# Kernel optimization log

Measured on AMD Instinct MI355X. Metric: run time of the kernel, lower is better.

## Reference

```python
import jax, jax.numpy as jnp
import numpy as np

B, N = 8, 1000
EMB, K, F1E, F1V, MSG = 4, 3, 2, 3, 2


def cross_concat(h):
    # h: [b, n, d] -> [b, n, n, 2d], interleaving (h_i, h_j) per feature (stack axis=-1 then reshape)
    b, n, d = h.shape
    hi = jnp.broadcast_to(h[:, :, None, :], (b, n, n, d))
    hj = jnp.broadcast_to(h[:, None, :, :], (b, n, n, d))
    return jnp.stack((hi, hj), axis=-1).reshape(b, n, n, 2 * d)


def setup_inputs() -> dict:
    key = jax.random.key(0)
    ks = jax.random.split(key, 16)
    p = lambda k, s: (jax.random.normal(k, s, dtype=jnp.float32) * 0.1)
    return {
        "x": jax.random.normal(ks[0], (B, N), dtype=jnp.float32),
        "W1_emb": p(ks[1], (1, EMB)), "b1_emb": p(ks[2], (EMB,)),
        "W2_emb": p(ks[3], (1, EMB)), "b2_emb": p(ks[4], (EMB,)),
        "W_f1e": p(ks[5], (2 * EMB, F1E)), "b_f1e": p(ks[6], (F1E,)),
        "W_f2e": p(ks[7], (2 * F1V, K)), "b_f2e": p(ks[8], (K,)),
        "W_fk": p(ks[9], (K, 2 * EMB, MSG)), "b_fk": p(ks[10], (K, MSG)),
        "W_f1v": p(ks[11], (F1E, F1V)), "b_f1v": p(ks[12], (F1V,)),
        "W_f2v": p(ks[13], (MSG + 1, 1)), "b_f2v": p(ks[14], (1,)),
    }


def reference(x, W1_emb, b1_emb, W2_emb, b2_emb, W_f1e, b_f1e, W_f2e, b_f2e,
              W_fk, b_fk, W_f1v, b_f1v, W_f2v, b_f2v):
    x_ = x[..., None]                                  # [B,N,1]
    h1 = x_ @ W1_emb + b1_emb                          # [B,N,EMB]
    c = cross_concat(h1)                               # [B,N,N,2*EMB]
    h = jnp.sum(c @ W_f1e + b_f1e, axis=2)             # [B,N,F1E]
    h2 = h @ W_f1v + b_f1v                             # [B,N,F1V]
    c2 = cross_concat(h2)                              # [B,N,N,2*F1V]
    hsum = jnp.sum(c2, axis=0)                         # [N,N,2*F1V] (sum over batch)
    edge_logits = hsum @ W_f2e + b_f2e                 # [N,N,K]
    edge_probs = jax.nn.softmax(edge_logits, axis=-1)  # [N,N,K]
    h1_ = x_ @ W2_emb + b2_emb                         # [B,N,EMB]
    c3 = cross_concat(h1_)                             # [B,N,N,2*EMB]
    # K per-relation edge MLPs, stacked on the last axis -> [B,N,N,MSG,K]
    messages = jnp.einsum('bijd,kdm->bijmk', c3, W_fk) + b_fk.T
    # softmax-weighted combine, summed over receiver axis j and relation axis k
    v_e = jnp.einsum('ijk,bijmk->bim', edge_probs, messages)  # [B,N,MSG]
    h2_ = x_ + (jnp.concatenate((v_e, x_), axis=-1) @ W_f2v + b_f2v)
    return jnp.squeeze(h2_, axis=-1)                   # [B,N]
```

## Files before the change

kernel.cpp:

```cpp
#include <hip/hip_runtime.h>

#define NN 1000
#define BB 8


__device__ __forceinline__ float wave_sum(float v) {
#pragma unroll
    for (int o = 32; o > 0; o >>= 1) v += __shfl_xor(v, o, 64);
    return v;
}

__global__ void prep_kernel(const float* __restrict__ x,
                            const float* __restrict__ W1, const float* __restrict__ b1,
                            const float* __restrict__ W2, const float* __restrict__ b2,
                            const float* __restrict__ Wf1e, const float* __restrict__ bf1e,
                            const float* __restrict__ Wf2e, const float* __restrict__ bf2e,
                            const float* __restrict__ Wfk, const float* __restrict__ bfk,
                            const float* __restrict__ Wf1v, const float* __restrict__ bf1v,
                            const float* __restrict__ Wf2v, const float* __restrict__ bf2v,
                            float* __restrict__ ws) {
    float* rec = ws;
    float* Ai  = ws + 12 * NN;
    float* XsT = ws + 16 * NN;
    float* cst = ws + 17 * NN;
    const int tid = threadIdx.x;

    __shared__ float s_part[4][8];
    __shared__ float s_small[6];

    float sx[8] = {0, 0, 0, 0, 0, 0, 0, 0};
    for (int j = tid; j < NN; j += 256) {
        float xs = 0.f;
#pragma unroll
        for (int b = 0; b < 8; ++b) {
            float v = x[b * NN + j];
            rec[j * 12 + 4 + b] = v;
            sx[b] += v;
            xs += v;
        }
        XsT[j] = xs;
    }
#pragma unroll
    for (int b = 0; b < 8; ++b) {
        float v = wave_sum(sx[b]);
        if ((tid & 63) == 0) s_part[tid >> 6][b] = v;
    }
    __syncthreads();

    if (tid == 0) {
        float Sx[8];
#pragma unroll
        for (int b = 0; b < 8; ++b)
            Sx[b] = s_part[0][b] + s_part[1][b] + s_part[2][b] + s_part[3][b];

        float alpha[2];
        for (int f = 0; f < 2; ++f) {
            float a = 0.f;
            for (int e = 0; e < 4; ++e) a += W1[e] * Wf1e[(2 * e) * 2 + f];
            alpha[f] = (float)NN * a;
        }
        float gamma[3];
        for (int v = 0; v < 3; ++v) {
            float g = 0.f;
            for (int f = 0; f < 2; ++f) g += alpha[f] * Wf1v[f * 3 + v];
            gamma[v] = g;
        }
        float Ds[3] = {0.f, 0.f, 0.f};
        for (int b = 0; b < 8; ++b) {
            float S1e[4];
            for (int e = 0; e < 4; ++e) S1e[e] = Sx[b] * W1[e] + (float)NN * b1[e];
            float beta[2];
            for (int f = 0; f < 2; ++f) {
                float t = 0.f;
                for (int e = 0; e < 4; ++e) t += b1[e] * Wf1e[(2 * e) * 2 + f];
                t *= (float)NN;
                for (int e = 0; e < 4; ++e) t += S1e[e] * Wf1e[(2 * e + 1) * 2 + f];
                t += (float)NN * bf1e[f];
                beta[f] = t;
            }
            for (int v = 0; v < 3; ++v) {
                float d = bf1v[v];
                for (int f = 0; f < 2; ++f) d += beta[f] * Wf1v[f * 3 + v];
                Ds[v] += d;
            }
        }
        for (int v = 0; v < 3; ++v) { s_small[v] = gamma[v]; s_small[3 + v] = Ds[v]; }

        for (int m = 0; m < 2; ++m)
            for (int k = 0; k < 3; ++k) {
                float uA = 0.f, uB = 0.f, vA = 0.f, vB = 0.f;
                for (int e = 0; e < 4; ++e) {
                    float wE = Wfk[k * 16 + (2 * e) * 2 + m];
                    float wO = Wfk[k * 16 + (2 * e + 1) * 2 + m];
                    uA += W2[e] * wE; uB += b2[e] * wE;
                    vA += W2[e] * wO; vB += b2[e] * wO;
                }
                cst[m * 3 + k]      = uA;
                cst[6 + m * 3 + k]  = uB + bfk[k * 2 + m] + vB;
                cst[12 + m * 3 + k] = vA;
            }
        cst[18] = Wf2v[0]; cst[19] = Wf2v[1]; cst[20] = Wf2v[2]; cst[21] = bf2v[0];
    }
    __syncthreads();

    const float g0 = s_small[0], g1 = s_small[1], g2 = s_small[2];
    const float d0 = s_small[3], d1 = s_small[4], d2 = s_small[5];
    for (int j = tid; j < NN; j += 256) {
        float xs = XsT[j];
        float H0 = g0 * xs + d0, H1 = g1 * xs + d1, H2 = g2 * xs + d2;
#pragma unroll
        for (int k = 0; k < 3; ++k) {
            Ai[j * 4 + k]   = H0 * Wf2e[0 * 3 + k] + H1 * Wf2e[2 * 3 + k] + H2 * Wf2e[4 * 3 + k] + bf2e[k];
            rec[j * 12 + k] = H0 * Wf2e[1 * 3 + k] + H1 * Wf2e[3 * 3 + k] + H2 * Wf2e[5 * 3 + k];
        }
        Ai[j * 4 + 3] = 0.f;
        rec[j * 12 + 3] = 0.f;
    }
}

__global__ __launch_bounds__(64) void main_kernel(const float* __restrict__ ws,
                                                  float* __restrict__ out) {
    const float* rec = ws;
    const float* Ai  = ws + 12 * NN;
    const float* cst = ws + 17 * NN;
    const int i = blockIdx.x;
    const int t = threadIdx.x;

    const float4 aif = *reinterpret_cast<const float4*>(Ai + i * 4);
    const float ai0 = aif.x, ai1 = aif.y, ai2 = aif.z;

    float Q0 = 0.f, Q1 = 0.f, Q2 = 0.f;
    float R[8][3];
#pragma unroll
    for (int b = 0; b < 8; ++b)
#pragma unroll
        for (int k = 0; k < 3; ++k) R[b][k] = 0.f;

    for (int j = t; j < NN; j += 64) {
        const float4 a  = *reinterpret_cast<const float4*>(rec + j * 12);
        const float4 xA = *reinterpret_cast<const float4*>(rec + j * 12 + 4);
        const float4 xB = *reinterpret_cast<const float4*>(rec + j * 12 + 8);
        float l0 = ai0 + a.x, l1 = ai1 + a.y, l2 = ai2 + a.z;
        float mx = fmaxf(l0, fmaxf(l1, l2));
        float e0 = __expf(l0 - mx), e1 = __expf(l1 - mx), e2 = __expf(l2 - mx);
        float inv = 1.f / (e0 + e1 + e2);
        float p0 = e0 * inv, p1 = e1 * inv, p2 = e2 * inv;
        Q0 += p0; Q1 += p1; Q2 += p2;
        float xv[8] = {xA.x, xA.y, xA.z, xA.w, xB.x, xB.y, xB.z, xB.w};
#pragma unroll
        for (int b = 0; b < 8; ++b) {
            R[b][0] += p0 * xv[b];
            R[b][1] += p1 * xv[b];
            R[b][2] += p2 * xv[b];
        }
    }

    Q0 = wave_sum(Q0); Q1 = wave_sum(Q1); Q2 = wave_sum(Q2);
#pragma unroll
    for (int b = 0; b < 8; ++b) {
        R[b][0] = wave_sum(R[b][0]);
        R[b][1] = wave_sum(R[b][1]);
        R[b][2] = wave_sum(R[b][2]);
    }

    if (t == 0) {
        float uA[6], cB[6], vA[6];
#pragma unroll
        for (int q = 0; q < 6; ++q) { uA[q] = cst[q]; cB[q] = cst[6 + q]; vA[q] = cst[12 + q]; }
        float w0 = cst[18], w1 = cst[19], w2 = cst[20], bf = cst[21];
        float Q[3] = {Q0, Q1, Q2};
#pragma unroll
        for (int b = 0; b < 8; ++b) {
            float xi = rec[i * 12 + 4 + b];
            float ve[2];
#pragma unroll
            for (int m = 0; m < 2; ++m) {
                float s = 0.f;
#pragma unroll
                for (int k = 0; k < 3; ++k)
                    s += Q[k] * (uA[m * 3 + k] * xi + cB[m * 3 + k]) + vA[m * 3 + k] * R[b][k];
                ve[m] = s;
            }
            out[b * NN + i] = xi + ve[0] * w0 + ve[1] * w1 + xi * w2 + bf;
        }
    }
}

extern "C" void kernel_launch(void* const* d_in, const int* in_sizes, int n_in,
                              void* d_out, int out_size, void* d_ws, size_t ws_size,
                              hipStream_t stream) {
    const float* x    = (const float*)d_in[0];
    const float* W1   = (const float*)d_in[1];
    const float* b1   = (const float*)d_in[2];
    const float* W2   = (const float*)d_in[3];
    const float* b2   = (const float*)d_in[4];
    const float* Wf1e = (const float*)d_in[5];
    const float* bf1e = (const float*)d_in[6];
    const float* Wf2e = (const float*)d_in[7];
    const float* bf2e = (const float*)d_in[8];
    const float* Wfk  = (const float*)d_in[9];
    const float* bfk  = (const float*)d_in[10];
    const float* Wf1v = (const float*)d_in[11];
    const float* bf1v = (const float*)d_in[12];
    const float* Wf2v = (const float*)d_in[13];
    const float* bf2v = (const float*)d_in[14];
    float* ws = (float*)d_ws;

    prep_kernel<<<1, 256, 0, stream>>>(x, W1, b1, W2, b2, Wf1e, bf1e, Wf2e, bf2e,
                                       Wfk, bfk, Wf1v, bf1v, Wf2v, bf2v, ws);
    main_kernel<<<NN, 64, 0, stream>>>(ws, (float*)d_out);
}
```

Before: 103.1 us.

## Fuse prep and main kernels into a single redundant-precompute kernel

Replaces the single-block prep kernel plus the per-row main kernel with one fused kernel. Each wave recomputes the global sum of x and the folded scalar constants itself, so the workspace round-trip and the serial one-block launch go away. The receiver-side logits are now derived algebraically from the per-column batch sum instead of being loaded from a precomputed record, and the final output is computed by 8 lanes in parallel instead of one. In exchange every wave redundantly reads all of x and recomputes the constants, and x is read with a strided per-batch layout in the inner loop.

Result: faster. 100.9 us (-2.1%).

```diff
diff --git a/kernel.cpp b/kernel.cpp
--- a/kernel.cpp
+++ b/kernel.cpp
@@ -1,8 +1,6 @@
 #include <hip/hip_runtime.h>
 
 #define NN 1000
-#define BB 8
-
 
 __device__ __forceinline__ float wave_sum(float v) {
 #pragma unroll
@@ -10,125 +8,102 @@
     return v;
 }
 
-__global__ void prep_kernel(const float* __restrict__ x,
-                            const float* __restrict__ W1, const float* __restrict__ b1,
-                            const float* __restrict__ W2, const float* __restrict__ b2,
-                            const float* __restrict__ Wf1e, const float* __restrict__ bf1e,
-                            const float* __restrict__ Wf2e, const float* __restrict__ bf2e,
-                            const float* __restrict__ Wfk, const float* __restrict__ bfk,
-                            const float* __restrict__ Wf1v, const float* __restrict__ bf1v,
-                            const float* __restrict__ Wf2v, const float* __restrict__ bf2v,
-                            float* __restrict__ ws) {
-    float* rec = ws;
-    float* Ai  = ws + 12 * NN;
-    float* XsT = ws + 16 * NN;
-    float* cst = ws + 17 * NN;
-    const int tid = threadIdx.x;
+__global__ __launch_bounds__(256) void fused_kernel(
+    const float* __restrict__ x,
+    const float* __restrict__ W1, const float* __restrict__ b1,
+    const float* __restrict__ W2, const float* __restrict__ b2,
+    const float* __restrict__ Wf1e, const float* __restrict__ bf1e,
+    const float* __restrict__ Wf2e, const float* __restrict__ bf2e,
+    const float* __restrict__ Wfk, const float* __restrict__ bfk,
+    const float* __restrict__ Wf1v, const float* __restrict__ bf1v,
+    const float* __restrict__ Wf2v, const float* __restrict__ bf2v,
+    float* __restrict__ out) {
+    const int wave = threadIdx.x >> 6;
+    const int lane = threadIdx.x & 63;
+    const int i = blockIdx.x * 4 + wave;
 
-    __shared__ float s_part[4][8];
-    __shared__ float s_small[6];
+    float s = 0.f;
+    const float4* x4 = reinterpret_cast<const float4*>(x);
+    for (int q = lane; q < 2 * NN; q += 64) {
+        float4 v = x4[q];
+        s += (v.x + v.y) + (v.z + v.w);
+    }
+    const float S = wave_sum(s);
 
-    float sx[8] = {0, 0, 0, 0, 0, 0, 0, 0};
-    for (int j = tid; j < NN; j += 256) {
-        float xs = 0.f;
+    float alpha[2];
 #pragma unroll
-        for (int b = 0; b < 8; ++b) {
-            float v = x[b * NN + j];
-            rec[j * 12 + 4 + b] = v;
-            sx[b] += v;
-            xs += v;
+    for (int f = 0; f < 2; ++f) {
+        float a = 0.f;
+#pragma unroll
+        for (int e = 0; e < 4; ++e) a += W1[e] * Wf1e[(2 * e) * 2 + f];
+        alpha[f] = (float)NN * a;
+    }
+    float gamma[3];
+#pragma unroll
+    for (int v = 0; v < 3; ++v) {
+        float g = 0.f;
+#pragma unroll
+        for (int f = 0; f < 2; ++f) g += alpha[f] * Wf1v[f * 3 + v];
+        gamma[v] = g;
+    }
+    float Bsum[2];
+#pragma unroll
+    for (int f = 0; f < 2; ++f) {
+        float t0 = 0.f, t1 = 0.f;
+#pragma unroll
+        for (int e = 0; e < 4; ++e) {
+            t0 += b1[e] * Wf1e[(2 * e) * 2 + f];
+            t1 += (S * W1[e] + 8.f * (float)NN * b1[e]) * Wf1e[(2 * e + 1) * 2 + f];
         }
-        XsT[j] = xs;
+        Bsum[f] = 8.f * (float)NN * t0 + t1 + 8.f * (float)NN * bf1e[f];
     }
+    float Ds[3];
 #pragma unroll
-    for (int b = 0; b < 8; ++b) {
-        float v = wave_sum(sx[b]);
-        if ((tid & 63) == 0) s_part[tid >> 6][b] = v;
+    for (int v = 0; v < 3; ++v) {
+        float d = 8.f * bf1v[v];
+#pragma unroll
+        for (int f = 0; f < 2; ++f) d += Bsum[f] * Wf1v[f * 3 + v];
+        Ds[v] = d;
     }
-    __syncthreads();
-
-    if (tid == 0) {
-        float Sx[8];
+    float PB[3], AiQ[3];
+    {
+        float xsi = 0.f;
 #pragma unroll
-        for (int b = 0; b < 8; ++b)
-            Sx[b] = s_part[0][b] + s_part[1][b] + s_part[2][b] + s_part[3][b];
-
-        float alpha[2];
-        for (int f = 0; f < 2; ++f) {
-            float a = 0.f;
-            for (int e = 0; e < 4; ++e) a += W1[e] * Wf1e[(2 * e) * 2 + f];
-            alpha[f] = (float)NN * a;
-        }
-        float gamma[3];
-        for (int v = 0; v < 3; ++v) {
-            float g = 0.f;
-            for (int f = 0; f < 2; ++f) g += alpha[f] * Wf1v[f * 3 + v];
-            gamma[v] = g;
-        }
-        float Ds[3] = {0.f, 0.f, 0.f};
-        for (int b = 0; b < 8; ++b) {
-            float S1e[4];
-            for (int e = 0; e < 4; ++e) S1e[e] = Sx[b] * W1[e] + (float)NN * b1[e];
-            float beta[2];
-            for (int f = 0; f < 2; ++f) {
-                float t = 0.f;
-                for (int e = 0; e < 4; ++e) t += b1[e] * Wf1e[(2 * e) * 2 + f];
-                t *= (float)NN;
-                for (int e = 0; e < 4; ++e) t += S1e[e] * Wf1e[(2 * e + 1) * 2 + f];
-                t += (float)NN * bf1e[f];
-                beta[f] = t;
-            }
-            for (int v = 0; v < 3; ++v) {
-                float d = bf1v[v];
-                for (int f = 0; f < 2; ++f) d += beta[f] * Wf1v[f * 3 + v];
-                Ds[v] += d;
-            }
-        }
-        for (int v = 0; v < 3; ++v) { s_small[v] = gamma[v]; s_small[3 + v] = Ds[v]; }
-
-        for (int m = 0; m < 2; ++m)
-            for (int k = 0; k < 3; ++k) {
-                float uA = 0.f, uB = 0.f, vA = 0.f, vB = 0.f;
-                for (int e = 0; e < 4; ++e) {
-                    float wE = Wfk[k * 16 + (2 * e) * 2 + m];
-                    float wO = Wfk[k * 16 + (2 * e + 1) * 2 + m];
-                    uA += W2[e] * wE; uB += b2[e] * wE;
-                    vA += W2[e] * wO; vB += b2[e] * wO;
-                }
-                cst[m * 3 + k]      = uA;
-                cst[6 + m * 3 + k]  = uB + bfk[k * 2 + m] + vB;
-                cst[12 + m * 3 + k] = vA;
-            }
-        cst[18] = Wf2v[0]; cst[19] = Wf2v[1]; cst[20] = Wf2v[2]; cst[21] = bf2v[0];
-    }
-    __syncthreads();
-
-    const float g0 = s_small[0], g1 = s_small[1], g2 = s_small[2];
-    const float d0 = s_small[3], d1 = s_small[4], d2 = s_small[5];
-    for (int j = tid; j < NN; j += 256) {
-        float xs = XsT[j];
-        float H0 = g0 * xs + d0, H1 = g1 * xs + d1, H2 = g2 * xs + d2;
+        for (int b = 0; b < 8; ++b) xsi += x[b * NN + i];
 #pragma unroll
         for (int k = 0; k < 3; ++k) {
-            Ai[j * 4 + k]   = H0 * Wf2e[0 * 3 + k] + H1 * Wf2e[2 * 3 + k] + H2 * Wf2e[4 * 3 + k] + bf2e[k];
-            rec[j * 12 + k] = H0 * Wf2e[1 * 3 + k] + H1 * Wf2e[3 * 3 + k] + H2 * Wf2e[5 * 3 + k];
+            float PA = 0.f, QA = 0.f, pb = 0.f, qb = 0.f;
+#pragma unroll
+            for (int v = 0; v < 3; ++v) {
+                PA += gamma[v] * Wf2e[(2 * v) * 3 + k];
+                QA += Ds[v]    * Wf2e[(2 * v) * 3 + k];
+                pb += gamma[v] * Wf2e[(2 * v + 1) * 3 + k];
+                qb += Ds[v]    * Wf2e[(2 * v + 1) * 3 + k];
+            }
+            PB[k]  = pb;
+            AiQ[k] = PA * xsi + QA + bf2e[k] + qb;
         }
-        Ai[j * 4 + 3] = 0.f;
-        rec[j * 12 + 3] = 0.f;
     }
-}
+    float uA[6], cB[6], vA[6];
+#pragma unroll
+    for (int m = 0; m < 2; ++m)
+#pragma unroll
+        for (int k = 0; k < 3; ++k) {
+            float ua = 0.f, ub = 0.f, va = 0.f, vb = 0.f;
+#pragma unroll
+            for (int e = 0; e < 4; ++e) {
+                float wE = Wfk[k * 16 + (2 * e) * 2 + m];
+                float wO = Wfk[k * 16 + (2 * e + 1) * 2 + m];
+                ua += W2[e] * wE; ub += b2[e] * wE;
+                va += W2[e] * wO; vb += b2[e] * wO;
+            }
+            uA[m * 3 + k] = ua;
+            cB[m * 3 + k] = ub + vb + bfk[k * 2 + m];
+            vA[m * 3 + k] = va;
+        }
 
-__global__ __launch_bounds__(64) void main_kernel(const float* __restrict__ ws,
-                                                  float* __restrict__ out) {
-    const float* rec = ws;
-    const float* Ai  = ws + 12 * NN;
-    const float* cst = ws + 17 * NN;
-    const int i = blockIdx.x;
-    const int t = threadIdx.x;
-
-    const float4 aif = *reinterpret_cast<const float4*>(Ai + i * 4);
-    const float ai0 = aif.x, ai1 = aif.y, ai2 = aif.z;
-
+    const float ai0 = AiQ[0], ai1 = AiQ[1], ai2 = AiQ[2];
+    const float pb0 = PB[0], pb1 = PB[1], pb2 = PB[2];
     float Q0 = 0.f, Q1 = 0.f, Q2 = 0.f;
     float R[8][3];
 #pragma unroll
@@ -136,17 +111,16 @@
 #pragma unroll
         for (int k = 0; k < 3; ++k) R[b][k] = 0.f;
 
-    for (int j = t; j < NN; j += 64) {
-        const float4 a  = *reinterpret_cast<const float4*>(rec + j * 12);
-        const float4 xA = *reinterpret_cast<const float4*>(rec + j * 12 + 4);
-        const float4 xB = *reinterpret_cast<const float4*>(rec + j * 12 + 8);
-        float l0 = ai0 + a.x, l1 = ai1 + a.y, l2 = ai2 + a.z;
+    for (int j = lane; j < NN; j += 64) {
+        float xv[8], xs = 0.f;
+#pragma unroll
+        for (int b = 0; b < 8; ++b) { xv[b] = x[b * NN + j]; xs += xv[b]; }
+        float l0 = ai0 + pb0 * xs, l1 = ai1 + pb1 * xs, l2 = ai2 + pb2 * xs;
         float mx = fmaxf(l0, fmaxf(l1, l2));
         float e0 = __expf(l0 - mx), e1 = __expf(l1 - mx), e2 = __expf(l2 - mx);
         float inv = 1.f / (e0 + e1 + e2);
         float p0 = e0 * inv, p1 = e1 * inv, p2 = e2 * inv;
         Q0 += p0; Q1 += p1; Q2 += p2;
-        float xv[8] = {xA.x, xA.y, xA.z, xA.w, xB.x, xB.y, xB.z, xB.w};
 #pragma unroll
         for (int b = 0; b < 8; ++b) {
             R[b][0] += p0 * xv[b];
@@ -163,26 +137,18 @@
         R[b][2] = wave_sum(R[b][2]);
     }
 
-    if (t == 0) {
-        float uA[6], cB[6], vA[6];
+    if (lane < 8) {
+        const int b = lane;
+        float xi = x[b * NN + i];
+        float Rk0 = R[b][0], Rk1 = R[b][1], Rk2 = R[b][2];
+        float ve[2];
 #pragma unroll
-        for (int q = 0; q < 6; ++q) { uA[q] = cst[q]; cB[q] = cst[6 + q]; vA[q] = cst[12 + q]; }
-        float w0 = cst[18], w1 = cst[19], w2 = cst[20], bf = cst[21];
-        float Q[3] = {Q0, Q1, Q2};
-#pragma unroll
-        for (int b = 0; b < 8; ++b) {
-            float xi = rec[i * 12 + 4 + b];
-            float ve[2];
-#pragma unroll
-            for (int m = 0; m < 2; ++m) {
-                float s = 0.f;
-#pragma unroll
-                for (int k = 0; k < 3; ++k)
-                    s += Q[k] * (uA[m * 3 + k] * xi + cB[m * 3 + k]) + vA[m * 3 + k] * R[b][k];
-                ve[m] = s;
-            }
-            out[b * NN + i] = xi + ve[0] * w0 + ve[1] * w1 + xi * w2 + bf;
+        for (int m = 0; m < 2; ++m) {
+            ve[m] = Q0 * (uA[m * 3 + 0] * xi + cB[m * 3 + 0]) + vA[m * 3 + 0] * Rk0
+                  + Q1 * (uA[m * 3 + 1] * xi + cB[m * 3 + 1]) + vA[m * 3 + 1] * Rk1
+                  + Q2 * (uA[m * 3 + 2] * xi + cB[m * 3 + 2]) + vA[m * 3 + 2] * Rk2;
         }
+        out[b * NN + i] = xi + ve[0] * Wf2v[0] + ve[1] * Wf2v[1] + xi * Wf2v[2] + bf2v[0];
     }
 }
 
@@ -204,9 +170,8 @@
     const float* bf1v = (const float*)d_in[12];
     const float* Wf2v = (const float*)d_in[13];
     const float* bf2v = (const float*)d_in[14];
-    float* ws = (float*)d_ws;
 
-    prep_kernel<<<1, 256, 0, stream>>>(x, W1, b1, W2, b2, Wf1e, bf1e, Wf2e, bf2e,
-                                       Wfk, bfk, Wf1v, bf1v, Wf2v, bf2v, ws);
-    main_kernel<<<NN, 64, 0, stream>>>(ws, (float*)d_out);
+    fused_kernel<<<NN / 4, 256, 0, stream>>>(x, W1, b1, W2, b2, Wf1e, bf1e,
+                                             Wf2e, bf2e, Wfk, bfk, Wf1v, bf1v,
+                                             Wf2v, bf2v, (float*)d_out);
 }
```
